# Optimization experiments

Measured on AMD Instinct MI355X. Metric: run time of the kernel, lower is better.

Reference implementation:

```python
import jax, jax.numpy as jnp
import numpy as np

B, S, D, H, EXPAND = 4, 2048, 256, 4, 4
DH = D // H
EPS = 1e-3  # keras BatchNormalization default epsilon
NEG = -1e9  # keras Softmax masking constant


def setup_inputs() -> dict:
    key = jax.random.key(0)
    ks = jax.random.split(key, 8)
    x = jax.random.normal(ks[0], (B, S, D), dtype=jnp.float32)
    mask = jax.random.randint(ks[1], (B, S), 0, 2) > 0
    mask = mask.at[:, 0].set(True)  # ensure each row has a valid token
    sc = 1.0 / np.sqrt(D)
    return {
        "x": x,
        "mask": mask,
        "bn1_gamma": jnp.ones((D,), jnp.float32),
        "bn1_beta": jnp.zeros((D,), jnp.float32),
        "bn1_mean": jax.random.normal(ks[2], (D,), jnp.float32) * 0.1,
        "bn1_var": jnp.ones((D,), jnp.float32),
        "qkv_w": jax.random.normal(ks[3], (D, 3 * D), jnp.float32) * sc,
        "proj_w": jax.random.normal(ks[4], (D, D), jnp.float32) * sc,
        "bn2_gamma": jnp.ones((D,), jnp.float32),
        "bn2_beta": jnp.zeros((D,), jnp.float32),
        "bn2_mean": jax.random.normal(ks[5], (D,), jnp.float32) * 0.1,
        "bn2_var": jnp.ones((D,), jnp.float32),
        "w1": jax.random.normal(ks[6], (D, EXPAND * D), jnp.float32) * sc,
        "w2": jax.random.normal(ks[7], (EXPAND * D, D), jnp.float32) * (sc / 2.0),
    }


def _bn(x, gamma, beta, mean, var):
    # inference-mode BatchNormalization over the channel axis
    return (x - mean) * jax.lax.rsqrt(var + EPS) * gamma + beta


def reference(x, mask, bn1_gamma, bn1_beta, bn1_mean, bn1_var, qkv_w, proj_w,
              bn2_gamma, bn2_beta, bn2_mean, bn2_var, w1, w2):
    scale = D ** (-0.5)
    # --- attention sub-block ---
    skip = x
    h = _bn(x, bn1_gamma, bn1_beta, bn1_mean, bn1_var)
    qkv = h @ qkv_w                                    # [B,S,3D]
    qkv = qkv.reshape(B, S, H, 3 * DH).transpose(0, 2, 1, 3)  # [B,H,S,3dh]
    q, k, v = qkv[..., :DH], qkv[..., DH:2 * DH], qkv[..., 2 * DH:]
    scores = jnp.einsum('bhqd,bhkd->bhqk', q, k) * scale      # [B,H,S,S]
    scores = scores + jnp.where(mask[:, None, None, :], 0.0, NEG)
    attn = jax.nn.softmax(scores, axis=-1)
    o = jnp.einsum('bhqk,bhkd->bhqd', attn, v)                # [B,H,S,dh]
    o = o.transpose(0, 2, 1, 3).reshape(B, S, D) @ proj_w
    x = o + skip
    # --- FFN sub-block ---
    skip = x
    h = _bn(x, bn2_gamma, bn2_beta, bn2_mean, bn2_var)
    h = jax.nn.swish(h @ w1)                                  # [B,S,4D]
    h = h @ w2
    return h + skip
```

## Files before the change

### kernel.cpp

```cpp
#include <hip/hip_runtime.h>
#include <math.h>

#define S_ 2048
#define D_ 256
#define B_ 4
#define H_ 4

typedef __attribute__((ext_vector_type(8))) short  bh8;
typedef __attribute__((ext_vector_type(4))) float  fx4;
typedef __attribute__((ext_vector_type(4))) unsigned short us4;
typedef __attribute__((ext_vector_type(4))) unsigned int   ux4;

__device__ inline unsigned short bf16r(float f) {
    unsigned int u = __builtin_bit_cast(unsigned int, f);
    return (unsigned short)((u + 0x7FFFu + ((u >> 16) & 1u)) >> 16);
}
__device__ inline unsigned int cvtpk(float a, float b) {
    unsigned int r;
    asm("v_cvt_pk_bf16_f32 %0, %1, %2" : "=v"(r) : "v"(a), "v"(b));
    return r;
}
__device__ inline float vexp2(float x) {
    float r;
    asm volatile("v_exp_f32 %0, %1\n\ts_nop 1" : "=v"(r) : "v"(x));
    return r;
}
__device__ inline void gl_lds16(const unsigned short* g, unsigned short* l) {
    __builtin_amdgcn_global_load_lds(
        (const __attribute__((address_space(1))) unsigned int*)g,
        (__attribute__((address_space(3))) unsigned int*)l, 16, 0, 0);
}
#define DRAIN_BARRIER() asm volatile("s_waitcnt vmcnt(0)\n\ts_barrier" ::: "memory")

__global__ __launch_bounds__(256) void prep_all_k(
    const float* __restrict__ qkv_w, const float* __restrict__ proj_w,
    const float* __restrict__ w1,    const float* __restrict__ w2,
    unsigned short* __restrict__ qkv_wt, unsigned short* __restrict__ proj_wt,
    unsigned short* __restrict__ w1t,    unsigned short* __restrict__ w2t,
    const float* __restrict__ x,
    const float* __restrict__ g1, const float* __restrict__ b1,
    const float* __restrict__ m1, const float* __restrict__ v1,
    unsigned short* __restrict__ xb,
    const int* __restrict__ mask, float* __restrict__ maskf)
{
    const int bidx = blockIdx.x;
    if (bidx < 768) {
        const float* W; unsigned short* Wt; int K, N, u0;
        if (bidx < 192)      { W = qkv_w;  Wt = qkv_wt;  K = 256;  N = 768;  u0 = bidx * 256; }
        else if (bidx < 256) { W = proj_w; Wt = proj_wt; K = 256;  N = 256;  u0 = (bidx - 192) * 256; }
        else if (bidx < 512) { W = w1;     Wt = w1t;     K = 256;  N = 1024; u0 = (bidx - 256) * 256; }
        else                 { W = w2;     Wt = w2t;     K = 1024; N = 256;  u0 = (bidx - 512) * 256; }
        const int u = u0 + threadIdx.x;
        const int k4 = u / N, n = u % N;
        us4 tv;
        #pragma unroll
        for (int j = 0; j < 4; ++j) tv[j] = bf16r(W[(size_t)(k4 * 4 + j) * N + n]);
        *(us4*)&Wt[(size_t)n * K + k4 * 4] = tv;
    } else if (bidx < 2816) {
        const int i = (bidx - 768) * 256 + threadIdx.x;
        const int c4 = (i & 63) * 4;
        float4 xv = *(const float4*)&x[(size_t)i * 4];
        float vv[4] = {xv.x, xv.y, xv.z, xv.w};
        us4 tv;
        #pragma unroll
        for (int j = 0; j < 4; ++j) {
            int c = c4 + j;
            float s = g1[c] * rsqrtf(v1[c] + 1e-3f);
            tv[j] = bf16r(vv[j] * s + (b1[c] - m1[c] * s));
        }
        *(us4*)&xb[(size_t)i * 4] = tv;
    } else {
        const int i = (bidx - 2816) * 256 + threadIdx.x;
        maskf[i] = mask[i] ? 0.0f : -1e9f;
    }
}

template<int BM, int E>
__global__ __launch_bounds__(256) void gemm_mfma_k(
    const unsigned short* __restrict__ A, const unsigned short* __restrict__ Wt,
    int N, int K,
    const float* __restrict__ res, float* __restrict__ outf,
    unsigned short* __restrict__ outb, unsigned short* __restrict__ kf_o,
    unsigned short* __restrict__ vf_o,
    const float* __restrict__ g2, const float* __restrict__ b2,
    const float* __restrict__ m2, const float* __restrict__ v2)
{
    constexpr int MI = BM / 32;
    constexpr int LA = BM / 32;
    __shared__ unsigned short Asb[2][BM * 64];
    __shared__ unsigned short Bsb[2][128 * 64];

    const int n0 = blockIdx.x * 128, m0 = blockIdx.y * BM;
    const int t = threadIdx.x, w = t >> 6, l = t & 63;
    const int qi = l & 15, g = l >> 4;
    const int wm = w >> 1, wn = w & 1;
    const int lr = l >> 3, lc = (l & 7) * 8;

    fx4 acc[MI][4];
    #pragma unroll
    for (int mi = 0; mi < MI; ++mi)
        #pragma unroll
        for (int ni = 0; ni < 4; ++ni) acc[mi][ni] = (fx4){0.f, 0.f, 0.f, 0.f};

    const int NT = K / 64;

#define STAGE(P, KT) {                                                        \
    const int kb = (KT) * 64;                                                 \
    _Pragma("unroll")                                                         \
    for (int i = 0; i < LA; ++i) {                                            \
        int r0 = (w * LA + i) * 8;                                            \
        gl_lds16(A + (size_t)(m0 + r0 + lr) * K + kb + lc, &Asb[P][r0 * 64]); \
    }                                                                         \
    _Pragma("unroll")                                                         \
    for (int i = 0; i < 4; ++i) {                                             \
        int r0 = (w * 4 + i) * 8;                                             \
        gl_lds16(Wt + (size_t)(n0 + r0 + lr) * K + kb + lc, &Bsb[P][r0 * 64]);\
    } }

    STAGE(0, 0);
    DRAIN_BARRIER();
    int p = 0;
    for (int kt = 0; kt < NT; ++kt) {
        if (kt + 1 < NT) STAGE(p ^ 1, kt + 1);
        #pragma unroll
        for (int kk = 0; kk < 2; ++kk) {
            bh8 af[MI], bf[4];
            #pragma unroll
            for (int mi = 0; mi < MI; ++mi)
                af[mi] = *(const bh8*)&Asb[p][(wm * (BM / 2) + mi * 16 + qi) * 64
                                             + kk * 32 + g * 8];
            #pragma unroll
            for (int ni = 0; ni < 4; ++ni)
                bf[ni] = *(const bh8*)&Bsb[p][(wn * 64 + ni * 16 + qi) * 64
                                             + kk * 32 + g * 8];
            #pragma unroll
            for (int mi = 0; mi < MI; ++mi)
                #pragma unroll
                for (int ni = 0; ni < 4; ++ni)
                    acc[mi][ni] = __builtin_amdgcn_mfma_f32_16x16x32_bf16(
                        af[mi], bf[ni], acc[mi][ni], 0, 0, 0);
        }
        DRAIN_BARRIER();
        p ^= 1;
    }
#undef STAGE

    const int mbase = m0 + wm * (BM / 2);
    #pragma unroll
    for (int ni = 0; ni < 4; ++ni) {
        const int nf = n0 + wn * 64 + ni * 16;
        if (E == 0) {
            const int h = nf / 192, rem = nf % 192;
            const int region = rem / 64;
            const int c = rem % 64 + qi;
            #pragma unroll
            for (int mi = 0; mi < MI; ++mi) {
                #pragma unroll
                for (int r = 0; r < 4; ++r) {
                    const int m = mbase + mi * 16 + g * 4 + r;
                    const int s = m & 2047;
                    const size_t bh = (size_t)((m >> 11) * 4 + h);
                    float a = acc[mi][ni][r];
                    if (region < 2) {
                        size_t off = (((bh * 128 + (s >> 4)) * 2 + (c >> 5)) * 64
                                      + ((c >> 3) & 3) * 16 + (s & 15)) * 8 + (c & 7);
                        if (region == 0)
                            outb[off] = bf16r(a * (0.0625f * 1.44269504f));
                        else
                            kf_o[off] = bf16r(a);
                    } else {
                        size_t off = ((((bh * 32 + (s >> 6)) * 4 + (c >> 4)) * 2
                                      + ((s >> 5) & 1)) * 64
                                      + ((s >> 3) & 3) * 16 + (c & 15)) * 8 + (s & 7);
                        vf_o[off] = bf16r(a);
                    }
                }
            }
        } else if (E == 1) {
            const int n = nf + qi;
            const float s2 = g2[n] * rsqrtf(v2[n] + 1e-3f);
            const float o2 = b2[n] - m2[n] * s2;
            #pragma unroll
            for (int mi = 0; mi < MI; ++mi) {
                #pragma unroll
                for (int r = 0; r < 4; ++r) {
                    const int m = mbase + mi * 16 + g * 4 + r;
                    const size_t idx = (size_t)m * N + n;
                    float rv = acc[mi][ni][r] + res[idx];
                    outf[idx] = rv;
                    outb[idx] = bf16r(rv * s2 + o2);
                }
            }
        } else if (E == 2) {
            const int n = nf + qi;
            #pragma unroll
            for (int mi = 0; mi < MI; ++mi) {
                #pragma unroll
                for (int r = 0; r < 4; ++r) {
                    const int m = mbase + mi * 16 + g * 4 + r;
                    float a = acc[mi][ni][r];
                    outb[(size_t)m * N + n] = bf16r(a / (1.0f + __expf(-a)));
                }
            }
        } else {
            const int n = nf + qi;
            #pragma unroll
            for (int mi = 0; mi < MI; ++mi) {
                #pragma unroll
                for (int r = 0; r < 4; ++r) {
                    const int m = mbase + mi * 16 + g * 4 + r;
                    const size_t idx = (size_t)m * N + n;
                    outf[idx] = acc[mi][ni][r] + res[idx];
                }
            }
        }
    }
}

__global__ __launch_bounds__(256) void attn_mfma_k(
    const unsigned short* __restrict__ qf,
    const unsigned short* __restrict__ kf,
    const unsigned short* __restrict__ vf,
    const float* __restrict__ maskf,
    unsigned short* __restrict__ ob)
{
    __shared__ fx4  Ol[2][64][8];
    __shared__ float Ll[2][64][2];

    const int bid = blockIdx.x;
    const int bh = bid & 15, qt = bid >> 4;
    const int b = bh >> 2, h = bh & 3;
    const int t = threadIdx.x;
    const int w = t >> 6, lane = t & 63;
    const int g = lane >> 4, qi = lane & 15;
    const int qh = w & 1;
    const int khalf = w >> 1;

    bh8 qA0, qA1, qB0, qB1;
    {
        const unsigned short* qp =
            qf + (size_t)(bh * 128 + qt * 4 + qh * 2) * 1024 + lane * 8;
        qA0 = *(const bh8*)(qp);
        qA1 = *(const bh8*)(qp + 512);
        qB0 = *(const bh8*)(qp + 1024);
        qB1 = *(const bh8*)(qp + 1536);
    }

    fx4 oA[4], oB[4];
    #pragma unroll
    for (int dt = 0; dt < 4; ++dt) {
        oA[dt] = (fx4){0.f, 0.f, 0.f, 0.f};
        oB[dt] = (fx4){0.f, 0.f, 0.f, 0.f};
    }
    float lsA = 0.f, lsB = 0.f;

    const unsigned short* kcur = kf + (size_t)bh * 131072 + khalf * 65536 + lane * 8;
    const unsigned short* vcur = vf + (size_t)bh * 131072 + khalf * 65536 + lane * 8;
    const float* mcur = maskf + b * 2048 + khalf * 1024 + g * 4;

    bh8 kfA[4][2], kfB[4][2], afA[4][2], afB[4][2];
    fx4 mvA[4], mvB[4];

#define LOADK(KF, MV) {                                                       \
    KF[0][0] = *(const bh8*)(kcur);        KF[0][1] = *(const bh8*)(kcur + 512);  \
    KF[1][0] = *(const bh8*)(kcur + 1024); KF[1][1] = *(const bh8*)(kcur + 1536); \
    KF[2][0] = *(const bh8*)(kcur + 2048); KF[2][1] = *(const bh8*)(kcur + 2560); \
    KF[3][0] = *(const bh8*)(kcur + 3072); KF[3][1] = *(const bh8*)(kcur + 3584); \
    MV[0] = *(const fx4*)(mcur);      MV[1] = *(const fx4*)(mcur + 16);       \
    MV[2] = *(const fx4*)(mcur + 32); MV[3] = *(const fx4*)(mcur + 48);       \
    kcur += 4096; mcur += 64; }

#define LOADV(AF) {                                                           \
    AF[0][0] = *(const bh8*)(vcur);        AF[0][1] = *(const bh8*)(vcur + 512);  \
    AF[1][0] = *(const bh8*)(vcur + 1024); AF[1][1] = *(const bh8*)(vcur + 1536); \
    AF[2][0] = *(const bh8*)(vcur + 2048); AF[2][1] = *(const bh8*)(vcur + 2560); \
    AF[3][0] = *(const bh8*)(vcur + 3072); AF[3][1] = *(const bh8*)(vcur + 3584); \
    vcur += 4096; }

#define PROCESS(KF, AF, MV) {                                                 \
    fx4 sA[4], sB[4];                                                         \
    _Pragma("unroll")                                                         \
    for (int kt = 0; kt < 4; ++kt) {                                          \
        fx4 zA = MV[kt];                                                      \
        zA = __builtin_amdgcn_mfma_f32_16x16x32_bf16(KF[kt][0], qA0, zA, 0, 0, 0); \
        zA = __builtin_amdgcn_mfma_f32_16x16x32_bf16(KF[kt][1], qA1, zA, 0, 0, 0); \
        sA[kt] = zA;                                                          \
        fx4 zB = MV[kt];                                                      \
        zB = __builtin_amdgcn_mfma_f32_16x16x32_bf16(KF[kt][0], qB0, zB, 0, 0, 0); \
        zB = __builtin_amdgcn_mfma_f32_16x16x32_bf16(KF[kt][1], qB1, zB, 0, 0, 0); \
        sB[kt] = zB;                                                          \
    }                                                                         \
    unsigned int pkA[4][2], pkB[4][2];                                        \
    _Pragma("unroll")                                                         \
    for (int kt = 0; kt < 4; ++kt) {                                          \
        float a0 = vexp2(sA[kt][0]);                                          \
        float a1 = vexp2(sA[kt][1]);                                          \
        float a2 = vexp2(sA[kt][2]);                                          \
        float a3 = vexp2(sA[kt][3]);                                          \
        lsA += (a0 + a1) + (a2 + a3);                                         \
        pkA[kt][0] = cvtpk(a0, a1);                                           \
        pkA[kt][1] = cvtpk(a2, a3);                                           \
        float b0 = vexp2(sB[kt][0]);                                          \
        float b1 = vexp2(sB[kt][1]);                                          \
        float b2 = vexp2(sB[kt][2]);                                          \
        float b3 = vexp2(sB[kt][3]);                                          \
        lsB += (b0 + b1) + (b2 + b3);                                         \
        pkB[kt][0] = cvtpk(b0, b1);                                           \
        pkB[kt][1] = cvtpk(b2, b3);                                           \
    }                                                                         \
    _Pragma("unroll")                                                         \
    for (int c = 0; c < 2; ++c) {                                             \
        unsigned int bwA[4], bwB[4];                                          \
        _Pragma("unroll")                                                     \
        for (int wd = 0; wd < 4; ++wd) {                                      \
            int src = (2 * (g & 1) + (wd >> 1)) * 16 + qi;                    \
            unsigned int vaA = (unsigned int)__shfl((int)pkA[2 * c][wd & 1], src, 64);     \
            unsigned int vbA = (unsigned int)__shfl((int)pkA[2 * c + 1][wd & 1], src, 64); \
            bwA[wd] = (g >= 2) ? vbA : vaA;                                   \
            unsigned int vaB = (unsigned int)__shfl((int)pkB[2 * c][wd & 1], src, 64);     \
            unsigned int vbB = (unsigned int)__shfl((int)pkB[2 * c + 1][wd & 1], src, 64); \
            bwB[wd] = (g >= 2) ? vbB : vaB;                                   \
        }                                                                     \
        bh8 bfA = __builtin_bit_cast(bh8, (ux4){bwA[0], bwA[1], bwA[2], bwA[3]}); \
        bh8 bfB = __builtin_bit_cast(bh8, (ux4){bwB[0], bwB[1], bwB[2], bwB[3]}); \
        _Pragma("unroll")                                                     \
        for (int dt = 0; dt < 4; ++dt) {                                      \
            oA[dt] = __builtin_amdgcn_mfma_f32_16x16x32_bf16(AF[dt][c], bfA, oA[dt], 0, 0, 0); \
            oB[dt] = __builtin_amdgcn_mfma_f32_16x16x32_bf16(AF[dt][c], bfB, oB[dt], 0, 0, 0); \
        }                                                                     \
    } }

    LOADK(kfA, mvA);
    LOADV(afA);
    for (int it = 0; it < 16; it += 2) {
        LOADK(kfB, mvB);
        LOADV(afB);
        PROCESS(kfA, afA, mvA);
        if (it + 2 < 16) {
            LOADK(kfA, mvA);
            LOADV(afA);
        }
        PROCESS(kfB, afB, mvB);
    }
#undef LOADK
#undef LOADV
#undef PROCESS

    const int slot = w & 1;
    if (w >= 2) {
        #pragma unroll
        for (int dt = 0; dt < 4; ++dt) {
            Ol[slot][lane][dt]     = oA[dt];
            Ol[slot][lane][4 + dt] = oB[dt];
        }
        Ll[slot][lane][0] = lsA;
        Ll[slot][lane][1] = lsB;
    }
    __syncthreads();
    if (w < 2) {
        lsA += Ll[slot][lane][0];
        lsB += Ll[slot][lane][1];
        #pragma unroll
        for (int dt = 0; dt < 4; ++dt) {
            fx4 pa = Ol[slot][lane][dt], pb = Ol[slot][lane][4 + dt];
            oA[dt][0] += pa[0]; oA[dt][1] += pa[1]; oA[dt][2] += pa[2]; oA[dt][3] += pa[3];
            oB[dt][0] += pb[0]; oB[dt][1] += pb[1]; oB[dt][2] += pb[2]; oB[dt][3] += pb[3];
        }
        lsA += __shfl_xor(lsA, 16, 64);
        lsA += __shfl_xor(lsA, 32, 64);
        lsB += __shfl_xor(lsB, 16, 64);
        lsB += __shfl_xor(lsB, 32, 64);
        float invA = 1.0f / lsA, invB = 1.0f / lsB;
        unsigned short* opA =
            ob + (size_t)(b * 2048 + qt * 64 + qh * 32 + qi) * 256 + h * 64 + g * 4;
        unsigned short* opB = opA + 16 * 256;
        #pragma unroll
        for (int dt = 0; dt < 4; ++dt) {
            us4 ta, tb;
            #pragma unroll
            for (int r = 0; r < 4; ++r) {
                ta[r] = bf16r(oA[dt][r] * invA);
                tb[r] = bf16r(oB[dt][r] * invB);
            }
            *(us4*)(opA + dt * 16) = ta;
            *(us4*)(opB + dt * 16) = tb;
        }
    }
}

extern "C" void kernel_launch(void* const* d_in, const int* in_sizes, int n_in,
                              void* d_out, int out_size, void* d_ws, size_t ws_size,
                              hipStream_t stream) {
    const float* x      = (const float*)d_in[0];
    const int*   mask   = (const int*)  d_in[1];
    const float* bn1_g  = (const float*)d_in[2];
    const float* bn1_b  = (const float*)d_in[3];
    const float* bn1_m  = (const float*)d_in[4];
    const float* bn1_v  = (const float*)d_in[5];
    const float* qkv_w  = (const float*)d_in[6];
    const float* proj_w = (const float*)d_in[7];
    const float* bn2_g  = (const float*)d_in[8];
    const float* bn2_b  = (const float*)d_in[9];
    const float* bn2_m  = (const float*)d_in[10];
    const float* bn2_v  = (const float*)d_in[11];
    const float* w1     = (const float*)d_in[12];
    const float* w2     = (const float*)d_in[13];
    float* out = (float*)d_out;

    char* w8 = (char*)d_ws;
    unsigned short* qkv_wt  = (unsigned short*)(w8 + 0);
    unsigned short* proj_wt = (unsigned short*)(w8 + 393216);
    unsigned short* w1t     = (unsigned short*)(w8 + 524288);
    unsigned short* w2t     = (unsigned short*)(w8 + 1048576);
    float*          maskf   = (float*)         (w8 + 1572864);
    unsigned short* xb      = (unsigned short*)(w8 + 2097152);
    float*          x2      = (float*)         (w8 + 6291456);
    unsigned short* x2nb    = (unsigned short*)(w8 + 14680064);
    unsigned short* qfrag   = (unsigned short*)(w8 + 18874368);
    unsigned short* kfrag   = (unsigned short*)(w8 + 23068672);
    unsigned short* vfrag   = (unsigned short*)(w8 + 27262976);
    unsigned short* ob      = (unsigned short*)(w8 + 31457280);
    unsigned short* h2b     = (unsigned short*)(w8 + 18874368);

    prep_all_k<<<2848, 256, 0, stream>>>(
        qkv_w, proj_w, w1, w2, qkv_wt, proj_wt, w1t, w2t,
        x, bn1_g, bn1_b, bn1_m, bn1_v, xb, mask, maskf);

    gemm_mfma_k<64, 0><<<dim3(6, 128), 256, 0, stream>>>(
        xb, qkv_wt, 768, 256, nullptr, nullptr, qfrag, kfrag, vfrag,
        nullptr, nullptr, nullptr, nullptr);

    attn_mfma_k<<<dim3(512), 256, 0, stream>>>(qfrag, kfrag, vfrag, maskf, ob);

    gemm_mfma_k<32, 1><<<dim3(2, 256), 256, 0, stream>>>(
        ob, proj_wt, 256, 256, x, x2, x2nb, nullptr, nullptr,
        bn2_g, bn2_b, bn2_m, bn2_v);

    gemm_mfma_k<64, 2><<<dim3(8, 128), 256, 0, stream>>>(
        x2nb, w1t, 1024, 256, nullptr, nullptr, h2b, nullptr, nullptr,
        nullptr, nullptr, nullptr, nullptr);

    gemm_mfma_k<32, 3><<<dim3(2, 256), 256, 0, stream>>>(
        h2b, w2t, 256, 1024, x2, out, nullptr, nullptr, nullptr,
        nullptr, nullptr, nullptr, nullptr);
}
```

Before: 102.9 us.

## Store GEMM operands in MFMA fragment layout and load directly without LDS

All GEMM operands (weights, normalized inputs, attention output, FFN hidden) are written in a pre-swizzled 16x32 MFMA fragment layout, so each wave can load its fragments straight from global memory with contiguous 16-byte loads. The GEMM becomes a single-wave 64x64 tile kernel with no shared memory staging, double buffering, or barriers. This removes LDS traffic and synchronization, but loses cross-wave reuse through LDS and relies on L2/cache for the repeated operand reads. Global-memory latency is also no longer hidden by software pipelining, and the scattered epilogue stores into the fragment layout may coalesce less well.

```diff
diff --git a/kernel.cpp b/kernel.cpp
--- a/kernel.cpp
+++ b/kernel.cpp
@@ -25,12 +25,11 @@
     asm volatile("v_exp_f32 %0, %1\n\ts_nop 1" : "=v"(r) : "v"(x));
     return r;
 }
-__device__ inline void gl_lds16(const unsigned short* g, unsigned short* l) {
-    __builtin_amdgcn_global_load_lds(
-        (const __attribute__((address_space(1))) unsigned int*)g,
-        (__attribute__((address_space(3))) unsigned int*)l, 16, 0, 0);
-}
-#define DRAIN_BARRIER() asm volatile("s_waitcnt vmcnt(0)\n\ts_barrier" ::: "memory")
+
+__device__ inline size_t fragoff(int m, int k, int K32) {
+    return ((size_t)(m >> 4) * K32 + (k >> 5)) * 512
+         + (size_t)((((k >> 3) & 3) * 16 + (m & 15)) * 8 + (k & 7));
+}
 
 __global__ __launch_bounds__(256) void prep_all_k(
     const float* __restrict__ qkv_w, const float* __restrict__ proj_w,
@@ -55,29 +54,29 @@
         us4 tv;
         #pragma unroll
         for (int j = 0; j < 4; ++j) tv[j] = bf16r(W[(size_t)(k4 * 4 + j) * N + n]);
-        *(us4*)&Wt[(size_t)n * K + k4 * 4] = tv;
+        *(us4*)&Wt[fragoff(n, k4 * 4, K >> 5)] = tv;
     } else if (bidx < 2816) {
         const int i = (bidx - 768) * 256 + threadIdx.x;
-        const int c4 = (i & 63) * 4;
+        const int m = i >> 6, c0 = (i & 63) * 4;
         float4 xv = *(const float4*)&x[(size_t)i * 4];
         float vv[4] = {xv.x, xv.y, xv.z, xv.w};
         us4 tv;
         #pragma unroll
         for (int j = 0; j < 4; ++j) {
-            int c = c4 + j;
+            int c = c0 + j;
             float s = g1[c] * rsqrtf(v1[c] + 1e-3f);
             tv[j] = bf16r(vv[j] * s + (b1[c] - m1[c] * s));
         }
-        *(us4*)&xb[(size_t)i * 4] = tv;
+        *(us4*)&xb[fragoff(m, c0, 8)] = tv;
     } else {
         const int i = (bidx - 2816) * 256 + threadIdx.x;
         maskf[i] = mask[i] ? 0.0f : -1e9f;
     }
 }
 
-template<int BM, int E>
-__global__ __launch_bounds__(256) void gemm_mfma_k(
-    const unsigned short* __restrict__ A, const unsigned short* __restrict__ Wt,
+template<int E>
+__global__ __launch_bounds__(64) void gemm_frag_k(
+    const unsigned short* __restrict__ Af, const unsigned short* __restrict__ Bf,
     int N, int K,
     const float* __restrict__ res, float* __restrict__ outf,
     unsigned short* __restrict__ outb, unsigned short* __restrict__ kf_o,
@@ -85,79 +84,49 @@
     const float* __restrict__ g2, const float* __restrict__ b2,
     const float* __restrict__ m2, const float* __restrict__ v2)
 {
-    constexpr int MI = BM / 32;
-    constexpr int LA = BM / 32;
-    __shared__ unsigned short Asb[2][BM * 64];
-    __shared__ unsigned short Bsb[2][128 * 64];
-
-    const int n0 = blockIdx.x * 128, m0 = blockIdx.y * BM;
-    const int t = threadIdx.x, w = t >> 6, l = t & 63;
+    const int l = threadIdx.x;
     const int qi = l & 15, g = l >> 4;
-    const int wm = w >> 1, wn = w & 1;
-    const int lr = l >> 3, lc = (l & 7) * 8;
-
-    fx4 acc[MI][4];
+    const int nt0 = blockIdx.x * 4, mt0 = blockIdx.y * 4;
+    const int K32 = K >> 5;
+
+    fx4 acc[4][4];
     #pragma unroll
-    for (int mi = 0; mi < MI; ++mi)
+    for (int mi = 0; mi < 4; ++mi)
         #pragma unroll
         for (int ni = 0; ni < 4; ++ni) acc[mi][ni] = (fx4){0.f, 0.f, 0.f, 0.f};
 
-    const int NT = K / 64;
-
-#define STAGE(P, KT) {                                                        \
-    const int kb = (KT) * 64;                                                 \
-    _Pragma("unroll")                                                         \
-    for (int i = 0; i < LA; ++i) {                                            \
-        int r0 = (w * LA + i) * 8;                                            \
-        gl_lds16(A + (size_t)(m0 + r0 + lr) * K + kb + lc, &Asb[P][r0 * 64]); \
-    }                                                                         \
-    _Pragma("unroll")                                                         \
-    for (int i = 0; i < 4; ++i) {                                             \
-        int r0 = (w * 4 + i) * 8;                                             \
-        gl_lds16(Wt + (size_t)(n0 + r0 + lr) * K + kb + lc, &Bsb[P][r0 * 64]);\
-    } }
-
-    STAGE(0, 0);
-    DRAIN_BARRIER();
-    int p = 0;
-    for (int kt = 0; kt < NT; ++kt) {
-        if (kt + 1 < NT) STAGE(p ^ 1, kt + 1);
-        #pragma unroll
-        for (int kk = 0; kk < 2; ++kk) {
-            bh8 af[MI], bf[4];
-            #pragma unroll
-            for (int mi = 0; mi < MI; ++mi)
-                af[mi] = *(const bh8*)&Asb[p][(wm * (BM / 2) + mi * 16 + qi) * 64
-                                             + kk * 32 + g * 8];
+    const unsigned short* Ab = Af + (size_t)mt0 * K32 * 512 + l * 8;
+    const unsigned short* Bb = Bf + (size_t)nt0 * K32 * 512 + l * 8;
+
+    #pragma unroll 2
+    for (int kt = 0; kt < K32; ++kt) {
+        bh8 af[4], bf[4];
+        #pragma unroll
+        for (int mi = 0; mi < 4; ++mi)
+            af[mi] = *(const bh8*)(Ab + ((size_t)mi * K32 + kt) * 512);
+        #pragma unroll
+        for (int ni = 0; ni < 4; ++ni)
+            bf[ni] = *(const bh8*)(Bb + ((size_t)ni * K32 + kt) * 512);
+        #pragma unroll
+        for (int mi = 0; mi < 4; ++mi)
             #pragma unroll
             for (int ni = 0; ni < 4; ++ni)
-                bf[ni] = *(const bh8*)&Bsb[p][(wn * 64 + ni * 16 + qi) * 64
-                                             + kk * 32 + g * 8];
-            #pragma unroll
-            for (int mi = 0; mi < MI; ++mi)
-                #pragma unroll
-                for (int ni = 0; ni < 4; ++ni)
-                    acc[mi][ni] = __builtin_amdgcn_mfma_f32_16x16x32_bf16(
-                        af[mi], bf[ni], acc[mi][ni], 0, 0, 0);
-        }
-        DRAIN_BARRIER();
-        p ^= 1;
-    }
-#undef STAGE
-
-    const int mbase = m0 + wm * (BM / 2);
+                acc[mi][ni] = __builtin_amdgcn_mfma_f32_16x16x32_bf16(
+                    af[mi], bf[ni], acc[mi][ni], 0, 0, 0);
+    }
+
     #pragma unroll
     for (int ni = 0; ni < 4; ++ni) {
-        const int nf = n0 + wn * 64 + ni * 16;
+        const int nf = (nt0 + ni) * 16;
         if (E == 0) {
             const int h = nf / 192, rem = nf % 192;
             const int region = rem / 64;
             const int c = rem % 64 + qi;
             #pragma unroll
-            for (int mi = 0; mi < MI; ++mi) {
+            for (int mi = 0; mi < 4; ++mi) {
                 #pragma unroll
                 for (int r = 0; r < 4; ++r) {
-                    const int m = mbase + mi * 16 + g * 4 + r;
+                    const int m = (mt0 + mi) * 16 + g * 4 + r;
                     const int s = m & 2047;
                     const size_t bh = (size_t)((m >> 11) * 4 + h);
                     float a = acc[mi][ni][r];
@@ -181,34 +150,34 @@
             const float s2 = g2[n] * rsqrtf(v2[n] + 1e-3f);
             const float o2 = b2[n] - m2[n] * s2;
             #pragma unroll
-            for (int mi = 0; mi < MI; ++mi) {
+            for (int mi = 0; mi < 4; ++mi) {
                 #pragma unroll
                 for (int r = 0; r < 4; ++r) {
-                    const int m = mbase + mi * 16 + g * 4 + r;
+                    const int m = (mt0 + mi) * 16 + g * 4 + r;
                     const size_t idx = (size_t)m * N + n;
                     float rv = acc[mi][ni][r] + res[idx];
                     outf[idx] = rv;
-                    outb[idx] = bf16r(rv * s2 + o2);
+                    outb[fragoff(m, n, 8)] = bf16r(rv * s2 + o2);
                 }
             }
         } else if (E == 2) {
             const int n = nf + qi;
             #pragma unroll
-            for (int mi = 0; mi < MI; ++mi) {
+            for (int mi = 0; mi < 4; ++mi) {
                 #pragma unroll
                 for (int r = 0; r < 4; ++r) {
-                    const int m = mbase + mi * 16 + g * 4 + r;
+                    const int m = (mt0 + mi) * 16 + g * 4 + r;
                     float a = acc[mi][ni][r];
-                    outb[(size_t)m * N + n] = bf16r(a / (1.0f + __expf(-a)));
+                    outb[fragoff(m, n, 32)] = bf16r(a / (1.0f + __expf(-a)));
                 }
             }
         } else {
             const int n = nf + qi;
             #pragma unroll
-            for (int mi = 0; mi < MI; ++mi) {
+            for (int mi = 0; mi < 4; ++mi) {
                 #pragma unroll
                 for (int r = 0; r < 4; ++r) {
-                    const int m = mbase + mi * 16 + g * 4 + r;
+                    const int m = (mt0 + mi) * 16 + g * 4 + r;
                     const size_t idx = (size_t)m * N + n;
                     outf[idx] = acc[mi][ni][r] + res[idx];
                 }
@@ -371,9 +340,7 @@
         lsB += __shfl_xor(lsB, 16, 64);
         lsB += __shfl_xor(lsB, 32, 64);
         float invA = 1.0f / lsA, invB = 1.0f / lsB;
-        unsigned short* opA =
-            ob + (size_t)(b * 2048 + qt * 64 + qh * 32 + qi) * 256 + h * 64 + g * 4;
-        unsigned short* opB = opA + 16 * 256;
+        const int mA = b * 2048 + qt * 64 + qh * 32 + qi;
         #pragma unroll
         for (int dt = 0; dt < 4; ++dt) {
             us4 ta, tb;
@@ -382,8 +349,9 @@
                 ta[r] = bf16r(oA[dt][r] * invA);
                 tb[r] = bf16r(oB[dt][r] * invB);
             }
-            *(us4*)(opA + dt * 16) = ta;
-            *(us4*)(opB + dt * 16) = tb;
+            const int n0 = h * 64 + dt * 16 + g * 4;
+            *(us4*)&ob[fragoff(mA,      n0, 8)] = ta;
+            *(us4*)&ob[fragoff(mA + 16, n0, 8)] = tb;
         }
     }
 }
@@ -426,21 +394,21 @@
         qkv_w, proj_w, w1, w2, qkv_wt, proj_wt, w1t, w2t,
         x, bn1_g, bn1_b, bn1_m, bn1_v, xb, mask, maskf);
 
-    gemm_mfma_k<64, 0><<<dim3(6, 128), 256, 0, stream>>>(
+    gemm_frag_k<0><<<dim3(12, 128), 64, 0, stream>>>(
         xb, qkv_wt, 768, 256, nullptr, nullptr, qfrag, kfrag, vfrag,
         nullptr, nullptr, nullptr, nullptr);
 
     attn_mfma_k<<<dim3(512), 256, 0, stream>>>(qfrag, kfrag, vfrag, maskf, ob);
 
-    gemm_mfma_k<32, 1><<<dim3(2, 256), 256, 0, stream>>>(
+    gemm_frag_k<1><<<dim3(4, 128), 64, 0, stream>>>(
         ob, proj_wt, 256, 256, x, x2, x2nb, nullptr, nullptr,
         bn2_g, bn2_b, bn2_m, bn2_v);
 
-    gemm_mfma_k<64, 2><<<dim3(8, 128), 256, 0, stream>>>(
+    gemm_frag_k<2><<<dim3(16, 128), 64, 0, stream>>>(
         x2nb, w1t, 1024, 256, nullptr, nullptr, h2b, nullptr, nullptr,
         nullptr, nullptr, nullptr, nullptr);
 
-    gemm_mfma_k<32, 3><<<dim3(2, 256), 256, 0, stream>>>(
+    gemm_frag_k<3><<<dim3(4, 128), 64, 0, stream>>>(
         h2b, w2t, 256, 1024, x2, out, nullptr, nullptr, nullptr,
         nullptr, nullptr, nullptr, nullptr);
 }
```

After: 107.7 us. 1.05x slower.

## Fuse projection, BN2, FFN up/down GEMMs into one per-row-tile kernel

Applied to the files above, without the earlier changes.

Replaces the three post-attention GEMM launches (proj+residual+BN2, w1+swish, w2+residual) with one kernel. Each 512-thread block owns 16 rows, keeps the normalized activations and the swish hidden tile in LDS, and reads MFMA-fragment-ordered weights straight from global memory. To support this, the attention output and the proj/w1/w2 weights are now written in a fragment-blocked layout. This removes the x2, x2nb and h2 global round trips and two launches. In exchange, weights are re-read from global/L2 by each of the 512 blocks without LDS staging, and each block has a small M tile.

```diff
diff --git a/kernel.cpp b/kernel.cpp
--- a/kernel.cpp
+++ b/kernel.cpp
@@ -32,11 +32,16 @@
 }
 #define DRAIN_BARRIER() asm volatile("s_waitcnt vmcnt(0)\n\ts_barrier" ::: "memory")
 
+__device__ inline size_t fragoff(int m, int k, int K32) {
+    return ((size_t)(m >> 4) * K32 + (k >> 5)) * 512
+         + (size_t)((((k >> 3) & 3) * 16 + (m & 15)) * 8 + (k & 7));
+}
+
 __global__ __launch_bounds__(256) void prep_all_k(
     const float* __restrict__ qkv_w, const float* __restrict__ proj_w,
     const float* __restrict__ w1,    const float* __restrict__ w2,
-    unsigned short* __restrict__ qkv_wt, unsigned short* __restrict__ proj_wt,
-    unsigned short* __restrict__ w1t,    unsigned short* __restrict__ w2t,
+    unsigned short* __restrict__ qkv_wt, unsigned short* __restrict__ proj_wf,
+    unsigned short* __restrict__ w1f,    unsigned short* __restrict__ w2f,
     const float* __restrict__ x,
     const float* __restrict__ g1, const float* __restrict__ b1,
     const float* __restrict__ m1, const float* __restrict__ v1,
@@ -45,17 +50,18 @@
 {
     const int bidx = blockIdx.x;
     if (bidx < 768) {
-        const float* W; unsigned short* Wt; int K, N, u0;
-        if (bidx < 192)      { W = qkv_w;  Wt = qkv_wt;  K = 256;  N = 768;  u0 = bidx * 256; }
-        else if (bidx < 256) { W = proj_w; Wt = proj_wt; K = 256;  N = 256;  u0 = (bidx - 192) * 256; }
-        else if (bidx < 512) { W = w1;     Wt = w1t;     K = 256;  N = 1024; u0 = (bidx - 256) * 256; }
-        else                 { W = w2;     Wt = w2t;     K = 1024; N = 256;  u0 = (bidx - 512) * 256; }
+        const float* W; unsigned short* Wt; int K, N, u0; bool frag;
+        if (bidx < 192)      { W = qkv_w;  Wt = qkv_wt; K = 256;  N = 768;  u0 = bidx * 256;        frag = false; }
+        else if (bidx < 256) { W = proj_w; Wt = proj_wf; K = 256;  N = 256;  u0 = (bidx - 192) * 256; frag = true; }
+        else if (bidx < 512) { W = w1;     Wt = w1f;    K = 256;  N = 1024; u0 = (bidx - 256) * 256; frag = true; }
+        else                 { W = w2;     Wt = w2f;    K = 1024; N = 256;  u0 = (bidx - 512) * 256; frag = true; }
         const int u = u0 + threadIdx.x;
         const int k4 = u / N, n = u % N;
         us4 tv;
         #pragma unroll
         for (int j = 0; j < 4; ++j) tv[j] = bf16r(W[(size_t)(k4 * 4 + j) * N + n]);
-        *(us4*)&Wt[(size_t)n * K + k4 * 4] = tv;
+        if (frag) *(us4*)&Wt[fragoff(n, k4 * 4, K >> 5)] = tv;
+        else      *(us4*)&Wt[(size_t)n * K + k4 * 4] = tv;
     } else if (bidx < 2816) {
         const int i = (bidx - 768) * 256 + threadIdx.x;
         const int c4 = (i & 63) * 4;
@@ -75,18 +81,13 @@
     }
 }
 
-template<int BM, int E>
-__global__ __launch_bounds__(256) void gemm_mfma_k(
+__global__ __launch_bounds__(256) void gemm_qkv_k(
     const unsigned short* __restrict__ A, const unsigned short* __restrict__ Wt,
-    int N, int K,
-    const float* __restrict__ res, float* __restrict__ outf,
-    unsigned short* __restrict__ outb, unsigned short* __restrict__ kf_o,
-    unsigned short* __restrict__ vf_o,
-    const float* __restrict__ g2, const float* __restrict__ b2,
-    const float* __restrict__ m2, const float* __restrict__ v2)
+    unsigned short* __restrict__ qf_o, unsigned short* __restrict__ kf_o,
+    unsigned short* __restrict__ vf_o)
 {
-    constexpr int MI = BM / 32;
-    constexpr int LA = BM / 32;
+    constexpr int BM = 64, MI = 2, LA = 2;
+    const int N = 768, K = 256;
     __shared__ unsigned short Asb[2][BM * 64];
     __shared__ unsigned short Bsb[2][128 * 64];
 
@@ -95,6 +96,7 @@
     const int qi = l & 15, g = l >> 4;
     const int wm = w >> 1, wn = w & 1;
     const int lr = l >> 3, lc = (l & 7) * 8;
+    (void)N;
 
     fx4 acc[MI][4];
     #pragma unroll
@@ -149,70 +151,136 @@
     #pragma unroll
     for (int ni = 0; ni < 4; ++ni) {
         const int nf = n0 + wn * 64 + ni * 16;
-        if (E == 0) {
-            const int h = nf / 192, rem = nf % 192;
-            const int region = rem / 64;
-            const int c = rem % 64 + qi;
+        const int h = nf / 192, rem = nf % 192;
+        const int region = rem / 64;
+        const int c = rem % 64 + qi;
+        #pragma unroll
+        for (int mi = 0; mi < MI; ++mi) {
             #pragma unroll
-            for (int mi = 0; mi < MI; ++mi) {
-                #pragma unroll
-                for (int r = 0; r < 4; ++r) {
-                    const int m = mbase + mi * 16 + g * 4 + r;
-                    const int s = m & 2047;
-                    const size_t bh = (size_t)((m >> 11) * 4 + h);
-                    float a = acc[mi][ni][r];
-                    if (region < 2) {
-                        size_t off = (((bh * 128 + (s >> 4)) * 2 + (c >> 5)) * 64
-                                      + ((c >> 3) & 3) * 16 + (s & 15)) * 8 + (c & 7);
-                        if (region == 0)
-                            outb[off] = bf16r(a * (0.0625f * 1.44269504f));
-                        else
-                            kf_o[off] = bf16r(a);
-                    } else {
-                        size_t off = ((((bh * 32 + (s >> 6)) * 4 + (c >> 4)) * 2
-                                      + ((s >> 5) & 1)) * 64
-                                      + ((s >> 3) & 3) * 16 + (c & 15)) * 8 + (s & 7);
-                        vf_o[off] = bf16r(a);
-                    }
+            for (int r = 0; r < 4; ++r) {
+                const int m = mbase + mi * 16 + g * 4 + r;
+                const int s = m & 2047;
+                const size_t bh = (size_t)((m >> 11) * 4 + h);
+                float a = acc[mi][ni][r];
+                if (region < 2) {
+                    size_t off = (((bh * 128 + (s >> 4)) * 2 + (c >> 5)) * 64
+                                  + ((c >> 3) & 3) * 16 + (s & 15)) * 8 + (c & 7);
+                    if (region == 0)
+                        qf_o[off] = bf16r(a * (0.0625f * 1.44269504f));
+                    else
+                        kf_o[off] = bf16r(a);
+                } else {
+                    size_t off = ((((bh * 32 + (s >> 6)) * 4 + (c >> 4)) * 2
+                                  + ((s >> 5) & 1)) * 64
+                                  + ((s >> 3) & 3) * 16 + (c & 15)) * 8 + (s & 7);
+                    vf_o[off] = bf16r(a);
                 }
             }
-        } else if (E == 1) {
-            const int n = nf + qi;
-            const float s2 = g2[n] * rsqrtf(v2[n] + 1e-3f);
-            const float o2 = b2[n] - m2[n] * s2;
+        }
+    }
+}
+
+__global__ __launch_bounds__(512) void fused_mlp_k(
+    const unsigned short* __restrict__ ob,
+    const unsigned short* __restrict__ proj_wf,
+    const unsigned short* __restrict__ w1f,
+    const unsigned short* __restrict__ w2f,
+    const float* __restrict__ x,
+    const float* __restrict__ g2, const float* __restrict__ b2,
+    const float* __restrict__ m2, const float* __restrict__ v2,
+    float* __restrict__ out)
+{
+    __shared__ unsigned short x2nb[8 * 512];
+    __shared__ unsigned short h2[32 * 512];
+
+    const int t = threadIdx.x, w = t >> 6, l = t & 63;
+    const int qi = l & 15, g = l >> 4;
+    const int mt = blockIdx.x;
+    const int m0 = mt * 16;
+
+    fx4 acc1[2];
+    acc1[0] = (fx4){0.f, 0.f, 0.f, 0.f};
+    acc1[1] = (fx4){0.f, 0.f, 0.f, 0.f};
+    {
+        const unsigned short* Ab = ob + (size_t)mt * 8 * 512 + l * 8;
+        const unsigned short* B0 = proj_wf + ((size_t)(w * 2 + 0) * 8) * 512 + l * 8;
+        const unsigned short* B1 = proj_wf + ((size_t)(w * 2 + 1) * 8) * 512 + l * 8;
+        #pragma unroll
+        for (int kt = 0; kt < 8; ++kt) {
+            bh8 a  = *(const bh8*)(Ab + (size_t)kt * 512);
+            bh8 b0 = *(const bh8*)(B0 + (size_t)kt * 512);
+            bh8 b1 = *(const bh8*)(B1 + (size_t)kt * 512);
+            acc1[0] = __builtin_amdgcn_mfma_f32_16x16x32_bf16(a, b0, acc1[0], 0, 0, 0);
+            acc1[1] = __builtin_amdgcn_mfma_f32_16x16x32_bf16(a, b1, acc1[1], 0, 0, 0);
+        }
+    }
+    float x2res[2][4];
+    #pragma unroll
+    for (int nt = 0; nt < 2; ++nt) {
+        const int n = w * 32 + nt * 16 + qi;
+        const float s2 = g2[n] * rsqrtf(v2[n] + 1e-3f);
+        const float o2 = b2[n] - m2[n] * s2;
+        #pragma unroll
+        for (int r = 0; r < 4; ++r) {
+            const int m = m0 + g * 4 + r;
+            float rv = acc1[nt][r] + x[(size_t)m * 256 + n];
+            x2res[nt][r] = rv;
+            x2nb[w * 512 + ((nt * 2 + (qi >> 3)) * 16 + g * 4 + r) * 8 + (qi & 7)]
+                = bf16r(rv * s2 + o2);
+        }
+    }
+    __syncthreads();
+
+    fx4 acc2[8];
+    #pragma unroll
+    for (int nt = 0; nt < 8; ++nt) acc2[nt] = (fx4){0.f, 0.f, 0.f, 0.f};
+    {
+        #pragma unroll
+        for (int kt = 0; kt < 8; ++kt) {
+            bh8 a = *(const bh8*)&x2nb[kt * 512 + l * 8];
             #pragma unroll
-            for (int mi = 0; mi < MI; ++mi) {
-                #pragma unroll
-                for (int r = 0; r < 4; ++r) {
-                    const int m = mbase + mi * 16 + g * 4 + r;
-                    const size_t idx = (size_t)m * N + n;
-                    float rv = acc[mi][ni][r] + res[idx];
-                    outf[idx] = rv;
-                    outb[idx] = bf16r(rv * s2 + o2);
-                }
+            for (int nt = 0; nt < 8; ++nt) {
+                bh8 b = *(const bh8*)(w1f + ((size_t)(w * 8 + nt) * 8 + kt) * 512 + l * 8);
+                acc2[nt] = __builtin_amdgcn_mfma_f32_16x16x32_bf16(a, b, acc2[nt], 0, 0, 0);
             }
-        } else if (E == 2) {
-            const int n = nf + qi;
-            #pragma unroll
-            for (int mi = 0; mi < MI; ++mi) {
-                #pragma unroll
-                for (int r = 0; r < 4; ++r) {
-                    const int m = mbase + mi * 16 + g * 4 + r;
-                    float a = acc[mi][ni][r];
-                    outb[(size_t)m * N + n] = bf16r(a / (1.0f + __expf(-a)));
-                }
-            }
-        } else {
-            const int n = nf + qi;
-            #pragma unroll
-            for (int mi = 0; mi < MI; ++mi) {
-                #pragma unroll
-                for (int r = 0; r < 4; ++r) {
-                    const int m = mbase + mi * 16 + g * 4 + r;
-                    const size_t idx = (size_t)m * N + n;
-                    outf[idx] = acc[mi][ni][r] + res[idx];
-                }
-            }
+        }
+    }
+    __syncthreads();
+    #pragma unroll
+    for (int nt = 0; nt < 8; ++nt) {
+        #pragma unroll
+        for (int r = 0; r < 4; ++r) {
+            const int n = w * 128 + nt * 16 + qi;
+            float a = acc2[nt][r];
+            float hv = a / (1.0f + __expf(-a));
+            h2[(n >> 5) * 512 + (((n >> 3) & 3) * 16 + g * 4 + r) * 8 + (n & 7)]
+                = bf16r(hv);
+        }
+    }
+    __syncthreads();
+
+    fx4 acc3[2];
+    acc3[0] = (fx4){0.f, 0.f, 0.f, 0.f};
+    acc3[1] = (fx4){0.f, 0.f, 0.f, 0.f};
+    {
+        const unsigned short* B0 = w2f + ((size_t)(w * 2 + 0) * 32) * 512 + l * 8;
+        const unsigned short* B1 = w2f + ((size_t)(w * 2 + 1) * 32) * 512 + l * 8;
+        #pragma unroll 4
+        for (int kt = 0; kt < 32; ++kt) {
+            bh8 a  = *(const bh8*)&h2[kt * 512 + l * 8];
+            bh8 b0 = *(const bh8*)(B0 + (size_t)kt * 512);
+            bh8 b1 = *(const bh8*)(B1 + (size_t)kt * 512);
+            acc3[0] = __builtin_amdgcn_mfma_f32_16x16x32_bf16(a, b0, acc3[0], 0, 0, 0);
+            acc3[1] = __builtin_amdgcn_mfma_f32_16x16x32_bf16(a, b1, acc3[1], 0, 0, 0);
+        }
+    }
+    #pragma unroll
+    for (int nt = 0; nt < 2; ++nt) {
+        #pragma unroll
+        for (int r = 0; r < 4; ++r) {
+            const int m = m0 + g * 4 + r;
+            const int n = w * 32 + nt * 16 + qi;
+            out[(size_t)m * 256 + n] = acc3[nt][r] + x2res[nt][r];
         }
     }
 }
@@ -371,9 +439,7 @@
         lsB += __shfl_xor(lsB, 16, 64);
         lsB += __shfl_xor(lsB, 32, 64);
         float invA = 1.0f / lsA, invB = 1.0f / lsB;
-        unsigned short* opA =
-            ob + (size_t)(b * 2048 + qt * 64 + qh * 32 + qi) * 256 + h * 64 + g * 4;
-        unsigned short* opB = opA + 16 * 256;
+        const int mA = b * 2048 + qt * 64 + qh * 32 + qi;
         #pragma unroll
         for (int dt = 0; dt < 4; ++dt) {
             us4 ta, tb;
@@ -382,8 +448,9 @@
                 ta[r] = bf16r(oA[dt][r] * invA);
                 tb[r] = bf16r(oB[dt][r] * invB);
             }
-            *(us4*)(opA + dt * 16) = ta;
-            *(us4*)(opB + dt * 16) = tb;
+            const int n0 = h * 64 + dt * 16 + g * 4;
+            *(us4*)&ob[fragoff(mA,      n0, 8)] = ta;
+            *(us4*)&ob[fragoff(mA + 16, n0, 8)] = tb;
         }
     }
 }
@@ -409,38 +476,25 @@
 
     char* w8 = (char*)d_ws;
     unsigned short* qkv_wt  = (unsigned short*)(w8 + 0);
-    unsigned short* proj_wt = (unsigned short*)(w8 + 393216);
-    unsigned short* w1t     = (unsigned short*)(w8 + 524288);
-    unsigned short* w2t     = (unsigned short*)(w8 + 1048576);
+    unsigned short* proj_wf = (unsigned short*)(w8 + 393216);
+    unsigned short* w1f     = (unsigned short*)(w8 + 524288);
+    unsigned short* w2f     = (unsigned short*)(w8 + 1048576);
     float*          maskf   = (float*)         (w8 + 1572864);
     unsigned short* xb      = (unsigned short*)(w8 + 2097152);
-    float*          x2      = (float*)         (w8 + 6291456);
-    unsigned short* x2nb    = (unsigned short*)(w8 + 14680064);
     unsigned short* qfrag   = (unsigned short*)(w8 + 18874368);
     unsigned short* kfrag   = (unsigned short*)(w8 + 23068672);
     unsigned short* vfrag   = (unsigned short*)(w8 + 27262976);
     unsigned short* ob      = (unsigned short*)(w8 + 31457280);
-    unsigned short* h2b     = (unsigned short*)(w8 + 18874368);
 
     prep_all_k<<<2848, 256, 0, stream>>>(
-        qkv_w, proj_w, w1, w2, qkv_wt, proj_wt, w1t, w2t,
+        qkv_w, proj_w, w1, w2, qkv_wt, proj_wf, w1f, w2f,
         x, bn1_g, bn1_b, bn1_m, bn1_v, xb, mask, maskf);
 
-    gemm_mfma_k<64, 0><<<dim3(6, 128), 256, 0, stream>>>(
-        xb, qkv_wt, 768, 256, nullptr, nullptr, qfrag, kfrag, vfrag,
-        nullptr, nullptr, nullptr, nullptr);
+    gemm_qkv_k<<<dim3(6, 128), 256, 0, stream>>>(
+        xb, qkv_wt, qfrag, kfrag, vfrag);
 
     attn_mfma_k<<<dim3(512), 256, 0, stream>>>(qfrag, kfrag, vfrag, maskf, ob);
 
-    gemm_mfma_k<32, 1><<<dim3(2, 256), 256, 0, stream>>>(
-        ob, proj_wt, 256, 256, x, x2, x2nb, nullptr, nullptr,
-        bn2_g, bn2_b, bn2_m, bn2_v);
-
-    gemm_mfma_k<64, 2><<<dim3(8, 128), 256, 0, stream>>>(
-        x2nb, w1t, 1024, 256, nullptr, nullptr, h2b, nullptr, nullptr,
-        nullptr, nullptr, nullptr, nullptr);
-
-    gemm_mfma_k<32, 3><<<dim3(2, 256), 256, 0, stream>>>(
-        h2b, w2t, 256, 1024, x2, out, nullptr, nullptr, nullptr,
-        nullptr, nullptr, nullptr, nullptr);
-}
+    fused_mlp_k<<<dim3(512), 512, 0, stream>>>(
+        ob, proj_wf, w1f, w2f, x, bn2_g, bn2_b, bn2_m, bn2_v, out);
+}
```

Result: faster. 88.93 us (-13.6%).
